# Kernel tuning notes

Measured on AMD Instinct MI355X. Metric: run time of the kernel, lower is better.

Reference implementation:

```python
import jax, jax.numpy as jnp
import numpy as np

PH = 8  # pool_height (init arg)


def _max_width(boxes_np, ph):
    # host-side replica of BidirectionalBoxPool._max_width (data-dependent output dim)
    b = np.asarray(boxes_np, dtype=np.float64)
    valid = ~np.all(b == 0, axis=-1)
    bw = np.where(valid, b[..., 2] - b[..., 0], 1.0)
    bh = np.where(valid, b[..., 3] - b[..., 1], 1.0)
    ratio = np.where(bw > bh, bw / bh, bh / bw)
    ratio = np.where(valid, ratio, 0.0)
    return int(np.ceil(ratio.max() * ph))


def _bilinear_sample(img, grid):
    # torch F.grid_sample defaults: bilinear, padding_mode='zeros', align_corners=False
    # img: (C,H,W); grid: (G,Wg,2) with grid[...,0]=x, grid[...,1]=y in [-1,1]
    C, H, W = img.shape
    ix = ((grid[..., 0] + 1.0) * W - 1.0) * 0.5
    iy = ((grid[..., 1] + 1.0) * H - 1.0) * 0.5
    x0 = jnp.floor(ix); y0 = jnp.floor(iy)
    x1 = x0 + 1.0;      y1 = y0 + 1.0

    def gather(xc, yc):
        m = ((xc >= 0) & (xc <= W - 1) & (yc >= 0) & (yc <= H - 1)).astype(img.dtype)
        xi = jnp.clip(xc, 0, W - 1).astype(jnp.int32)
        yi = jnp.clip(yc, 0, H - 1).astype(jnp.int32)
        return img[:, yi, xi] * m  # (C,G,Wg)

    w00 = (x1 - ix) * (y1 - iy); w10 = (ix - x0) * (y1 - iy)
    w01 = (x1 - ix) * (iy - y0); w11 = (ix - x0) * (iy - y0)
    return (gather(x0, y0) * w00 + gather(x1, y0) * w10 +
            gather(x0, y1) * w01 + gather(x1, y1) * w11)


def _forward(x, boxes, max_width):
    N, C, H, W = x.shape
    K = boxes.shape[1]
    dt = x.dtype
    xmin, ymin, xmax, ymax = boxes[..., 0], boxes[..., 1], boxes[..., 2], boxes[..., 3]
    valid = ~((xmin == 0) & (ymin == 0) & (xmax == 0) & (ymax == 0))  # (N,K)
    bw = jnp.where(valid, xmax - xmin, 1.0)
    bh = jnp.where(valid, ymax - ymin, 1.0)
    wide = bw > bh  # wide -> _make_grid_wide, else _make_grid_tall
    width = jnp.ceil(jnp.where(wide, bw / bh, bh / bw) * PH).astype(jnp.int32)
    width = jnp.where(valid, width, 0)               # (N,K) per-box sample count
    wf = jnp.maximum(width, 2).astype(dt)            # safe denominator (width-1)

    ii = jnp.arange(PH, dtype=dt)[:, None]           # (PH,1) pool rows
    jj = jnp.arange(max_width, dtype=dt)[None, :]    # (1,MW) pool cols
    bc = lambda a: a[..., None, None]                # (N,K,1,1)
    xm, ym, bwb, bhb, wfb, wideb = bc(xmin), bc(ymin), bc(bw), bc(bh), bc(wf), bc(wide)

    def coords(i, j):
        # wide: x varies with j over [xmin,xmax], y with i over [ymin,ymax]
        gx_w = (xm + j * bwb / (wfb - 1.0) - W / 2) / (W / 2)
        gy_w = (ym + i * bhb / (PH - 1.0) - H / 2) / (H / 2)
        # tall: x varies with i, y = ymin + (height - j)*each_w (per original code)
        gx_t = (xm + i * bwb / (PH - 1.0) - W / 2) / (W / 2)
        gy_t = (ym + (wfb - j) * bhb / (wfb - 1.0) - H / 2) / (H / 2)
        return jnp.where(wideb, gx_w, gx_t), jnp.where(wideb, gy_w, gy_t)

    mask = jnp.arange(max_width)[None, None, None, :] < width[..., None, None]  # (N,K,1,MW)
    gx0, gy0 = coords(ii, jj)                         # forward grid
    gx1, gy1 = coords(PH - 1.0 - ii, wfb - 1.0 - jj)  # grid.flip((0,1)) within valid cols
    g0 = jnp.where(mask[..., None], jnp.stack(jnp.broadcast_arrays(gx0, gy0), -1), -2.0)
    g1 = jnp.where(mask[..., None], jnp.stack(jnp.broadcast_arrays(gx1, gy1), -1), -2.0)
    grids = jnp.stack([g0, g1], axis=2)               # (N,K,2,PH,MW,2)

    flat = grids.reshape(N, K * 2 * PH, max_width, 2)
    sampled = jax.vmap(_bilinear_sample)(x, flat)     # (N,C,K*2*PH,MW)
    feats = sampled.reshape(N, C, K, 2, PH, max_width).transpose(0, 2, 3, 1, 4, 5)
    widths = jnp.broadcast_to(width.astype(dt)[..., None], (N, K, 2))
    return feats, widths


def setup_inputs() -> dict:
    N, K, C, H, W = 8, 64, 128, 128, 128
    key = jax.random.key(0)
    x = jax.random.normal(key, (N, C, H, W), dtype=jnp.float32)
    rng = np.random.default_rng(0)
    bwn = rng.uniform(8.0, 64.0, (N, K))
    bhn = rng.uniform(8.0, 16.0, (N, K))
    x0 = rng.uniform(0.0, 1.0, (N, K)) * (W - 1 - bwn)
    y0 = rng.uniform(0.0, 1.0, (N, K)) * (H - 1 - bhn)
    boxes = np.stack([x0, y0, x0 + bwn, y0 + bhn], -1).astype(np.float32)
    boxes[:, -2:, :] = 0.0  # a couple of 'empty' boxes per image (skipped)
    return {"x": x, "boxes": jnp.asarray(boxes)}


def reference(x, boxes):
    mw = _max_width(np.asarray(boxes), PH)  # static, data-dependent output width
    return _forward(x, boxes, mw)
```

## Files before the change

kernel.cpp:

```cpp
#include <hip/hip_runtime.h>


namespace {
constexpr int kN = 8, kK = 64, kC = 128, kH = 128, kW = 128, kPH = 8;
constexpr int kHW = kH * kW;

__global__ __launch_bounds__(256) void boxpool_kernel(
    const float* __restrict__ x,
    const float* __restrict__ boxes,
    float* __restrict__ out,
    const int MW)
{
  const int b = blockIdx.x;
  const int nk = b >> 1;
  const int chalf = b & 1;
  const int n = nk >> 6;
  const int tid = threadIdx.x;

  const int bb = nk * 4;
  const float xmin = boxes[bb + 0];
  const float ymin = boxes[bb + 1];
  const float xmax = boxes[bb + 2];
  const float ymax = boxes[bb + 3];
  const bool valid = !(xmin == 0.f && ymin == 0.f && xmax == 0.f && ymax == 0.f);
  const float bw = valid ? (xmax - xmin) : 1.f;
  const float bh = valid ? (ymax - ymin) : 1.f;
  const bool wide = bw > bh;
  const float ratio = wide ? (bw / bh) : (bh / bw);
  const int width = valid ? (int)ceilf(ratio * 8.f) : 0;
  const float wf = fmaxf((float)width, 2.f);
  const int wm = width < MW ? width : MW;

  const int points = kPH * MW;
  const size_t feats_sz = (size_t)kN * kK * 2 * kC * points;

  if (chalf == 0 && tid == 0) {
    float2 wv; wv.x = (float)width; wv.y = (float)width;
    *reinterpret_cast<float2*>(out + feats_sz + (size_t)nk * 2) = wv;
  }

  const float* __restrict__ xn = x + ((size_t)n * kC + (size_t)chalf * 64) * kHW;
  float* __restrict__ out0 = out + ((size_t)(nk * 2 + 0) * kC + (size_t)chalf * 64) * points;
  float* __restrict__ out1 = out + ((size_t)(nk * 2 + 1) * kC + (size_t)chalf * 64) * points;

  const int pairs = points >> 1;
  for (int pp = tid; pp < pairs; pp += 256) {
    int   off[8];
    float wgt[8];
    int   e1[2];

#pragma unroll
    for (int s = 0; s < 2; ++s) {
      const int p = 2 * pp + s;
      const int i = p / MW;
      const int j = p - i * MW;
      const int jp = (j < wm) ? (wm - 1 - j) : j;
      e1[s] = (kPH - 1 - i) * MW + jp;

      float w00 = 0.f, w10 = 0.f, w01 = 0.f, w11 = 0.f;
      int   o00 = 0, o10 = 0, o01 = 0, o11 = 0;
      if (j < wm) {
        const float jf = (float)j, iff = (float)i;
        float gx, gy;
        if (wide) {
          gx = (xmin + (jf * bw) / (wf - 1.f) - 64.f) / 64.f;
          gy = (ymin + (iff * bh) / 7.f - 64.f) / 64.f;
        } else {
          gx = (xmin + (iff * bw) / 7.f - 64.f) / 64.f;
          gy = (ymin + ((wf - jf) * bh) / (wf - 1.f) - 64.f) / 64.f;
        }
        const float ix = ((gx + 1.f) * 128.f - 1.f) * 0.5f;
        const float iy = ((gy + 1.f) * 128.f - 1.f) * 0.5f;
        const float x0 = floorf(ix), y0 = floorf(iy);
        const float wx1 = ix - x0, wx0 = (x0 + 1.f) - ix;
        const float wy1 = iy - y0, wy0 = (y0 + 1.f) - iy;
        const int xi = (int)x0, yi = (int)y0;
        const bool xb0 = (xi >= 0) && (xi <= kW - 1);
        const bool xb1 = (xi + 1 >= 0) && (xi + 1 <= kW - 1);
        const bool yb0 = (yi >= 0) && (yi <= kH - 1);
        const bool yb1 = (yi + 1 >= 0) && (yi + 1 <= kH - 1);
        const int x0c = min(max(xi, 0), kW - 1);
        const int x1c = min(max(xi + 1, 0), kW - 1);
        const int y0c = min(max(yi, 0), kH - 1);
        const int y1c = min(max(yi + 1, 0), kH - 1);
        o00 = y0c * kW + x0c; o10 = y0c * kW + x1c;
        o01 = y1c * kW + x0c; o11 = y1c * kW + x1c;
        w00 = (xb0 && yb0) ? wx0 * wy0 : 0.f;
        w10 = (xb1 && yb0) ? wx1 * wy0 : 0.f;
        w01 = (xb0 && yb1) ? wx0 * wy1 : 0.f;
        w11 = (xb1 && yb1) ? wx1 * wy1 : 0.f;
      }
      off[4 * s + 0] = o00; off[4 * s + 1] = o10;
      off[4 * s + 2] = o01; off[4 * s + 3] = o11;
      wgt[4 * s + 0] = w00; wgt[4 * s + 1] = w10;
      wgt[4 * s + 2] = w01; wgt[4 * s + 3] = w11;
    }

#pragma unroll 4
    for (int c = 0; c < 64; ++c) {
      const float* __restrict__ plc = xn + (size_t)c * kHW;
      const float vA = wgt[0] * plc[off[0]] + wgt[1] * plc[off[1]]
                     + wgt[2] * plc[off[2]] + wgt[3] * plc[off[3]];
      const float vB = wgt[4] * plc[off[4]] + wgt[5] * plc[off[5]]
                     + wgt[6] * plc[off[6]] + wgt[7] * plc[off[7]];
      float* o0c = out0 + (size_t)c * points;
      float2 v2; v2.x = vA; v2.y = vB;
      *reinterpret_cast<float2*>(o0c + 2 * pp) = v2;
      float* o1c = out1 + (size_t)c * points;
      o1c[e1[0]] = vA;
      o1c[e1[1]] = vB;
    }
  }
}
}

extern "C" void kernel_launch(void* const* d_in, const int* in_sizes, int n_in,
                              void* d_out, int out_size, void* d_ws, size_t ws_size,
                              hipStream_t stream) {
  (void)in_sizes; (void)n_in; (void)d_ws; (void)ws_size;
  const float* x = (const float*)d_in[0];
  const float* boxes = (const float*)d_in[1];
  float* out = (float*)d_out;

  const long long widths_elems = (long long)kN * kK * 2;
  const long long per_mw = (long long)kN * kK * 2 * kC * kPH;
  const int MW = (int)(((long long)out_size - widths_elems) / per_mw);

  boxpool_kernel<<<dim3(kN * kK * 2), dim3(256), 0, stream>>>(x, boxes, out, MW);
}
```

Baseline: 397.8 us.

## Restrict gather work to active box columns and zero-fill padding separately

Each block now iterates only over the sample points inside the box's actual width (wm) instead of all MW padded columns. The padded tail is written with a separate vectorised zero-fill loop. Threads are split across channel groups when the active point count is small, so all 256 threads stay busy on narrow boxes. This cuts redundant gathers and arithmetic for the many boxes much narrower than the maximum width, at the cost of more branching and an extra store pass over the tail.

```diff
diff --git a/kernel.cpp b/kernel.cpp
--- a/kernel.cpp
+++ b/kernel.cpp
@@ -35,80 +35,129 @@
   const size_t feats_sz = (size_t)kN * kK * 2 * kC * points;
 
   if (chalf == 0 && tid == 0) {
-    float2 wv; wv.x = (float)width; wv.y = (float)width;
-    *reinterpret_cast<float2*>(out + feats_sz + (size_t)nk * 2) = wv;
+    out[feats_sz + (size_t)nk * 2 + 0] = (float)width;
+    out[feats_sz + (size_t)nk * 2 + 1] = (float)width;
   }
 
   const float* __restrict__ xn = x + ((size_t)n * kC + (size_t)chalf * 64) * kHW;
   float* __restrict__ out0 = out + ((size_t)(nk * 2 + 0) * kC + (size_t)chalf * 64) * points;
   float* __restrict__ out1 = out + ((size_t)(nk * 2 + 1) * kC + (size_t)chalf * 64) * points;
 
-  const int pairs = points >> 1;
-  for (int pp = tid; pp < pairs; pp += 256) {
-    int   off[8];
-    float wgt[8];
-    int   e1[2];
+  const int cp2 = (wm + 1) >> 1;
+  const int Pact = kPH * cp2;
+  const bool mwEven = (MW & 1) == 0;
+
+  if (Pact > 0) {
+    int Pp, cpl;
+    if (Pact <= 64)       { Pp = 64;  cpl = 16; }
+    else if (Pact <= 128) { Pp = 128; cpl = 32; }
+    else                  { Pp = 256; cpl = 64; }
+    const int pid0 = tid % Pp;
+    const int c0   = (tid / Pp) * cpl;
+
+    for (int pid = pid0; pid < Pact; pid += Pp) {
+      const int i   = pid / cp2;
+      const int ja2 = pid - i * cp2;
+      const int j0  = 2 * ja2;
+      const bool hasS1 = (j0 + 1 < MW);
+
+      int   off[8];
+      float wgt[8];
+      int   e1[2];
 
 #pragma unroll
-    for (int s = 0; s < 2; ++s) {
-      const int p = 2 * pp + s;
-      const int i = p / MW;
-      const int j = p - i * MW;
-      const int jp = (j < wm) ? (wm - 1 - j) : j;
-      e1[s] = (kPH - 1 - i) * MW + jp;
+      for (int s = 0; s < 2; ++s) {
+        const int j = j0 + s;
+        const bool inRow = (s == 0) || hasS1;
+        const int jc = inRow ? j : 0;
+        const int jp = (jc < wm) ? (wm - 1 - jc) : jc;
+        e1[s] = (kPH - 1 - i) * MW + jp;
 
-      float w00 = 0.f, w10 = 0.f, w01 = 0.f, w11 = 0.f;
-      int   o00 = 0, o10 = 0, o01 = 0, o11 = 0;
-      if (j < wm) {
-        const float jf = (float)j, iff = (float)i;
-        float gx, gy;
-        if (wide) {
-          gx = (xmin + (jf * bw) / (wf - 1.f) - 64.f) / 64.f;
-          gy = (ymin + (iff * bh) / 7.f - 64.f) / 64.f;
+        float w00 = 0.f, w10 = 0.f, w01 = 0.f, w11 = 0.f;
+        int   o00 = 0, o10 = 0, o01 = 0, o11 = 0;
+        if (inRow && j < wm) {
+          const float jf = (float)j, iff = (float)i;
+          float gx, gy;
+          if (wide) {
+            gx = (xmin + (jf * bw) / (wf - 1.f) - 64.f) / 64.f;
+            gy = (ymin + (iff * bh) / 7.f - 64.f) / 64.f;
+          } else {
+            gx = (xmin + (iff * bw) / 7.f - 64.f) / 64.f;
+            gy = (ymin + ((wf - jf) * bh) / (wf - 1.f) - 64.f) / 64.f;
+          }
+          const float ix = ((gx + 1.f) * 128.f - 1.f) * 0.5f;
+          const float iy = ((gy + 1.f) * 128.f - 1.f) * 0.5f;
+          const float x0 = floorf(ix), y0 = floorf(iy);
+          const float wx1 = ix - x0, wx0 = (x0 + 1.f) - ix;
+          const float wy1 = iy - y0, wy0 = (y0 + 1.f) - iy;
+          const int xi = (int)x0, yi = (int)y0;
+          const bool xb0 = (xi >= 0) && (xi <= kW - 1);
+          const bool xb1 = (xi + 1 >= 0) && (xi + 1 <= kW - 1);
+          const bool yb0 = (yi >= 0) && (yi <= kH - 1);
+          const bool yb1 = (yi + 1 >= 0) && (yi + 1 <= kH - 1);
+          const int x0c = min(max(xi, 0), kW - 1);
+          const int x1c = min(max(xi + 1, 0), kW - 1);
+          const int y0c = min(max(yi, 0), kH - 1);
+          const int y1c = min(max(yi + 1, 0), kH - 1);
+          o00 = y0c * kW + x0c; o10 = y0c * kW + x1c;
+          o01 = y1c * kW + x0c; o11 = y1c * kW + x1c;
+          w00 = (xb0 && yb0) ? wx0 * wy0 : 0.f;
+          w10 = (xb1 && yb0) ? wx1 * wy0 : 0.f;
+          w01 = (xb0 && yb1) ? wx0 * wy1 : 0.f;
+          w11 = (xb1 && yb1) ? wx1 * wy1 : 0.f;
+        }
+        off[4 * s + 0] = o00; off[4 * s + 1] = o10;
+        off[4 * s + 2] = o01; off[4 * s + 3] = o11;
+        wgt[4 * s + 0] = w00; wgt[4 * s + 1] = w10;
+        wgt[4 * s + 2] = w01; wgt[4 * s + 3] = w11;
+      }
+
+      const int base0 = i * MW + j0;
+      const int cend = c0 + cpl;
+#pragma unroll 4
+      for (int c = c0; c < cend; ++c) {
+        const float* __restrict__ plc = xn + (size_t)c * kHW;
+        const float vA = wgt[0] * plc[off[0]] + wgt[1] * plc[off[1]]
+                       + wgt[2] * plc[off[2]] + wgt[3] * plc[off[3]];
+        const float vB = wgt[4] * plc[off[4]] + wgt[5] * plc[off[5]]
+                       + wgt[6] * plc[off[6]] + wgt[7] * plc[off[7]];
+        float* o0c = out0 + (size_t)c * points;
+        float* o1c = out1 + (size_t)c * points;
+        if (hasS1) {
+          if (mwEven) {
+            float2 v2; v2.x = vA; v2.y = vB;
+            *reinterpret_cast<float2*>(o0c + base0) = v2;
+          } else {
+            o0c[base0] = vA;
+            o0c[base0 + 1] = vB;
+          }
+          o1c[e1[0]] = vA;
+          o1c[e1[1]] = vB;
         } else {
-          gx = (xmin + (iff * bw) / 7.f - 64.f) / 64.f;
-          gy = (ymin + ((wf - jf) * bh) / (wf - 1.f) - 64.f) / 64.f;
+          o0c[base0] = vA;
+          o1c[e1[0]] = vA;
         }
-        const float ix = ((gx + 1.f) * 128.f - 1.f) * 0.5f;
-        const float iy = ((gy + 1.f) * 128.f - 1.f) * 0.5f;
-        const float x0 = floorf(ix), y0 = floorf(iy);
-        const float wx1 = ix - x0, wx0 = (x0 + 1.f) - ix;
-        const float wy1 = iy - y0, wy0 = (y0 + 1.f) - iy;
-        const int xi = (int)x0, yi = (int)y0;
-        const bool xb0 = (xi >= 0) && (xi <= kW - 1);
-        const bool xb1 = (xi + 1 >= 0) && (xi + 1 <= kW - 1);
-        const bool yb0 = (yi >= 0) && (yi <= kH - 1);
-        const bool yb1 = (yi + 1 >= 0) && (yi + 1 <= kH - 1);
-        const int x0c = min(max(xi, 0), kW - 1);
-        const int x1c = min(max(xi + 1, 0), kW - 1);
-        const int y0c = min(max(yi, 0), kH - 1);
-        const int y1c = min(max(yi + 1, 0), kH - 1);
-        o00 = y0c * kW + x0c; o10 = y0c * kW + x1c;
-        o01 = y1c * kW + x0c; o11 = y1c * kW + x1c;
-        w00 = (xb0 && yb0) ? wx0 * wy0 : 0.f;
-        w10 = (xb1 && yb0) ? wx1 * wy0 : 0.f;
-        w01 = (xb0 && yb1) ? wx0 * wy1 : 0.f;
-        w11 = (xb1 && yb1) ? wx1 * wy1 : 0.f;
       }
-      off[4 * s + 0] = o00; off[4 * s + 1] = o10;
-      off[4 * s + 2] = o01; off[4 * s + 3] = o11;
-      wgt[4 * s + 0] = w00; wgt[4 * s + 1] = w10;
-      wgt[4 * s + 2] = w01; wgt[4 * s + 3] = w11;
     }
+  }
 
-#pragma unroll 4
-    for (int c = 0; c < 64; ++c) {
-      const float* __restrict__ plc = xn + (size_t)c * kHW;
-      const float vA = wgt[0] * plc[off[0]] + wgt[1] * plc[off[1]]
-                     + wgt[2] * plc[off[2]] + wgt[3] * plc[off[3]];
-      const float vB = wgt[4] * plc[off[4]] + wgt[5] * plc[off[5]]
-                     + wgt[6] * plc[off[6]] + wgt[7] * plc[off[7]];
-      float* o0c = out0 + (size_t)c * points;
-      float2 v2; v2.x = vA; v2.y = vB;
-      *reinterpret_cast<float2*>(o0c + 2 * pp) = v2;
-      float* o1c = out1 + (size_t)c * points;
-      o1c[e1[0]] = vA;
-      o1c[e1[1]] = vB;
+  const int ja0 = 2 * cp2;
+  const int dl  = MW - ja0;
+  if (dl > 0) {
+    for (int r = tid; r < 2 * 64 * kPH; r += 256) {
+      const int dir = r & 1;
+      const int c   = (r >> 1) & 63;
+      const int i   = r >> 7;
+      float* base = (dir ? out1 : out0) + (size_t)c * points + i * MW + ja0;
+      int t = 0;
+      int head = (int)((4 - ((((uintptr_t)base) >> 2) & 3)) & 3);
+      head = head < dl ? head : dl;
+      for (; t < head; ++t) base[t] = 0.f;
+      for (; t + 4 <= dl; t += 4) {
+        float4 z; z.x = 0.f; z.y = 0.f; z.z = 0.f; z.w = 0.f;
+        *reinterpret_cast<float4*>(base + t) = z;
+      }
+      for (; t < dl; ++t) base[t] = 0.f;
     }
   }
 }
```

Result: slower. 562.6 us (+41.4%).
